# Kernel optimization log

Measured on AMD Instinct MI355X. Metric: run time of the kernel, lower is better.

## Reference

```python
import jax, jax.numpy as jnp
import numpy as np

NUM_HEADS = 16

def rotate_half(x):
    h = x.shape[-1] // 2
    return jnp.concatenate([-x[..., h:], x[..., :h]], axis=-1)

def setup_inputs() -> dict:
    key = jax.random.key(0)
    k1, k2, k3 = jax.random.split(key, 3)
    B, S, H = 2, 2048, 1024
    x = jax.random.normal(k1, (B, S, H), dtype=jnp.float32)
    W_qkv = jax.random.normal(k2, (3 * H, H), dtype=jnp.float32) * (1.0 / np.sqrt(H))
    W_proj = jax.random.normal(k3, (H, H), dtype=jnp.float32) * (1.0 / np.sqrt(H))
    return {"x": x, "W_qkv": W_qkv, "W_proj": W_proj}

def reference(x, W_qkv, W_proj):
    B, S, H = x.shape
    nH = NUM_HEADS
    hd = H // nH
    # QKV projection (bias=False): y = x @ W.T
    qkv = jnp.einsum('bsh,oh->bso', x, W_qkv)  # [B,S,3H]
    q, k, v = jnp.split(qkv, 3, axis=-1)
    def to_heads(t):
        return t.reshape(B, S, nH, hd).transpose(0, 2, 1, 3)  # [B,nH,S,hd]
    q, k, v = to_heads(q), to_heads(k), to_heads(v)
    # RoPE on first half of head_dim; freqs dim = hd//2
    half = hd // 2
    inv_freq = 1.0 / (10000.0 ** (jnp.arange(0, hd, 2, dtype=jnp.float32) / hd))  # [hd//2]
    t = jnp.arange(S, dtype=jnp.float32)
    freqs = t[:, None] * inv_freq[None, :]  # [S, hd//2]
    cos = jnp.cos(freqs)[None, None]  # [1,1,S,hd//2]
    sin = jnp.sin(freqs)[None, None]
    q_half, q_rest = q[..., :half], q[..., half:]
    k_half, k_rest = k[..., :half], k[..., half:]
    q_rot = q_half * cos + rotate_half(q_half) * sin
    k_rot = k_half * cos + rotate_half(k_half) * sin
    q = jnp.concatenate([q_rot, q_rest], axis=-1)
    k = jnp.concatenate([k_rot, k_rest], axis=-1)
    # scaled dot-product attention (no mask, dropout=0 / eval)
    scale = 1.0 / np.sqrt(hd)
    att = jnp.einsum('bhqd,bhkd->bhqk', q, k) * scale  # [B,nH,S,S]
    att = jax.nn.softmax(att, axis=-1)
    out = jnp.einsum('bhqk,bhkd->bhqd', att, v)  # [B,nH,S,hd]
    out = out.transpose(0, 2, 1, 3).reshape(B, S, H)
    return jnp.einsum('bsh,oh->bso', out, W_proj)
```

## Files before the change

### kernel.cpp

```cpp
#include <hip/hip_runtime.h>
#include <math.h>

#define SEQ  2048
#define NHD  16
#define HD   64
#define HDIM 1024

typedef short s16x8 __attribute__((ext_vector_type(8)));
typedef short s16x4 __attribute__((ext_vector_type(4)));
typedef float f32x4 __attribute__((ext_vector_type(4)));

typedef const __attribute__((address_space(1))) unsigned int* gp_t;
typedef __attribute__((address_space(3))) unsigned int* lp_t;

__device__ __forceinline__ void async16(const short* g, short* l) {
    __builtin_amdgcn_global_load_lds((gp_t)g, (lp_t)l, 16, 0, 0);
}

__device__ __forceinline__ short f2bf(float f) {
    unsigned int u = __float_as_uint(f);
    u += 0x7fff + ((u >> 16) & 1);
    return (short)(u >> 16);
}
__device__ __forceinline__ float bf2f(short s) {
    return __uint_as_float(((unsigned int)(unsigned short)s) << 16);
}
__device__ __forceinline__ unsigned pkbf(float a, float b) {
    unsigned ua = __float_as_uint(a) + 0x8000u;
    unsigned ub = __float_as_uint(b) + 0x8000u;
    return __builtin_amdgcn_perm(ua, ub, 0x03020706u);
}

#define XG4  (4096 * 1024 / 4)
#define WQG4 (3072 * 1024 / 4)
#define WPG4 (1024 * 1024 / 4)
#define NCVT ((XG4 + WQG4 + WPG4) / 256)
__global__ void cvt_rope_k(const void* __restrict__ xr, const void* __restrict__ wqr,
                           const void* __restrict__ wpr, short* __restrict__ xo,
                           short* __restrict__ wqo, short* __restrict__ wpo,
                           float2* __restrict__ tab) {
    const int tid = threadIdx.x;
    if (blockIdx.x >= NCVT) {
        int i = (blockIdx.x - NCVT) * 256 + tid;
        int s = i >> 5, d = i & 31;
        float invf = (float)pow(10000.0, -(double)d / 32.0);
        float af = (float)s * invf;
        tab[i] = make_float2((float)cos((double)af), (float)sin((double)af));
        return;
    }
    int i = blockIdx.x * 256 + tid;
    const void* in; short* out; int j;
    if (i < XG4)             { in = xr;  out = xo;  j = i; }
    else if (i < XG4 + WQG4) { in = wqr; out = wqo; j = i - XG4; }
    else                     { in = wpr; out = wpo; j = i - XG4 - WQG4; }
    const int jbase = j - tid;
    unsigned short h = ((const unsigned short*)in)[(size_t)jbase * 4 + tid];
    int e = (h >> 7) & 0xFF;
    unsigned long long b = __ballot(e >= 100 && e <= 140);
    __shared__ int tot;
    if (tid == 0) tot = 0;
    __syncthreads();
    if ((tid & 63) == 0) atomicAdd(&tot, __popcll(b));
    __syncthreads();
    if (tot > 230) {
        ((s16x4*)out)[j] = ((const s16x4*)in)[j];
    } else {
        f32x4 v = ((const f32x4*)in)[j];
        union { unsigned u[2]; s16x4 v; } r;
        r.u[0] = pkbf(v[0], v[1]);
        r.u[1] = pkbf(v[2], v[3]);
        ((s16x4*)out)[j] = r.v;
    }
}

template<int MODE>
__global__ __launch_bounds__(256, 2)
void gemm_bt(const short* __restrict__ A, const short* __restrict__ B,
             short* __restrict__ q, short* __restrict__ kbuf, short* __restrict__ vt,
             float* __restrict__ C, const float2* __restrict__ tab,
             int K, int N) {
    __shared__ __align__(16) short As[2][128 * 32];
    __shared__ __align__(16) short Bs[2][128 * 32];
    const int tid  = threadIdx.x;
    const int w    = tid >> 6, lane = tid & 63;
    const int quad = lane >> 4, l16 = lane & 15;
    const int wm = (w >> 1) * 64, wn = (w & 1) * 64;
    const int rowA0 = blockIdx.y * 128;
    const int colB0 = blockIdx.x * 128;

    auto stage = [&](int buf, int kb) {
        #pragma unroll
        for (int i = 0; i < 2; ++i) {
            int cidx = i * 256 + w * 64 + lane;
            int row = cidx >> 2, sc = cidx & 3;
            int c = sc ^ (row & 3);
            async16(&A[(long)(rowA0 + row) * K + kb + c * 8],
                    &As[buf][(i * 256 + w * 64) * 8]);
            async16(&B[(long)(colB0 + row) * K + kb + c * 8],
                    &Bs[buf][(i * 256 + w * 64) * 8]);
        }
    };

    f32x4 acc[4][4] = {};
    stage(0, 0);

    for (int kb = 0, it = 0; kb < K; kb += 32, ++it) {
        const int cur = it & 1;
        __syncthreads();
        if (kb + 32 < K) stage(cur ^ 1, kb + 32);

        s16x8 af[4], bfr[4];
        const int slot = quad ^ (l16 & 3);
        #pragma unroll
        for (int mi = 0; mi < 4; ++mi)
            af[mi] = *(const s16x8*)&As[cur][(wm + mi * 16 + l16) * 32 + slot * 8];
        #pragma unroll
        for (int ni = 0; ni < 4; ++ni)
            bfr[ni] = *(const s16x8*)&Bs[cur][(wn + ni * 16 + l16) * 32 + slot * 8];
        #pragma unroll
        for (int mi = 0; mi < 4; ++mi)
            #pragma unroll
            for (int ni = 0; ni < 4; ++ni)
                acc[mi][ni] = __builtin_amdgcn_mfma_f32_16x16x32_bf16(
                    af[mi], bfr[ni], acc[mi][ni], 0, 0, 0);
    }

    const int cb = colB0 + wn;
    if (MODE == 1) {
        #pragma unroll
        for (int mi = 0; mi < 4; ++mi) {
            #pragma unroll
            for (int r = 0; r < 4; ++r) {
                int gm = rowA0 + wm + mi * 16 + quad * 4 + r;
                float* cp = C + (long)gm * N + cb + l16;
                #pragma unroll
                for (int ni = 0; ni < 4; ++ni)
                    cp[ni * 16] = acc[mi][ni][r];
            }
        }
        return;
    }
    const int sector = cb >> 10;
    const int head   = (cb & 1023) >> 6;
    const int gmb = rowA0 + wm;
    const int b = gmb >> 11, s0 = gmb & 2047;
    __syncthreads();
    short* arena = (w < 2) ? (&As[0][0] + w * 4096) : (&Bs[0][0] + (w - 2) * 4096);
    auto aw = [&](int row, int col, short val) {
        arena[row * 64 + (((col >> 3) ^ (row & 7)) << 3) + (col & 7)] = val;
    };
    if (sector < 2) {
        const float sc = (sector == 0) ? 0.18033688f : 1.0f;
        #pragma unroll
        for (int mi = 0; mi < 4; ++mi) {
            #pragma unroll
            for (int r = 0; r < 4; ++r) {
                int lrow = mi * 16 + quad * 4 + r;
                int s = s0 + lrow;
                float v0 = acc[mi][0][r], v1 = acc[mi][1][r];
                float v2 = acc[mi][2][r], v3 = acc[mi][3][r];
                float2 cs0 = tab[s * 32 + l16];
                float2 cs1 = tab[s * 32 + 16 + l16];
                float n0 = v0 * cs0.x - v1 * cs0.y;
                float n1 = v1 * cs1.x + v0 * cs1.y;
                aw(lrow, l16,      f2bf(n0 * sc));
                aw(lrow, l16 + 16, f2bf(n1 * sc));
                aw(lrow, l16 + 32, f2bf(v2 * sc));
                aw(lrow, l16 + 48, f2bf(v3 * sc));
            }
        }
        short* dst0 = (sector == 0 ? q : kbuf)
                    + ((long)((b * NHD + head) * SEQ + s0)) * HD;
        #pragma unroll
        for (int it = 0; it < 8; ++it) {
            int row = it * 8 + (lane >> 3), cc = lane & 7;
            s16x8 vv = *(const s16x8*)&arena[row * 64 + ((cc ^ (row & 7)) << 3)];
            *(s16x8*)&dst0[row * HD + cc * 8] = vv;
        }
    } else {
        #pragma unroll
        for (int mi = 0; mi < 4; ++mi) {
            #pragma unroll
            for (int r = 0; r < 4; ++r) {
                int scol = mi * 16 + quad * 4 + r;
                aw(l16,      scol, f2bf(acc[mi][0][r]));
                aw(l16 + 16, scol, f2bf(acc[mi][1][r]));
                aw(l16 + 32, scol, f2bf(acc[mi][2][r]));
                aw(l16 + 48, scol, f2bf(acc[mi][3][r]));
            }
        }
        short* dstv = vt + ((long)((b * NHD + head) * HD)) * SEQ + s0;
        #pragma unroll
        for (int it = 0; it < 8; ++it) {
            int dd = it * 8 + (lane >> 3), so8 = lane & 7;
            s16x8 vv = *(const s16x8*)&arena[dd * 64 + ((so8 ^ (dd & 7)) << 3)];
            *(s16x8*)&dstv[(long)dd * SEQ + so8 * 8] = vv;
        }
    }
}

__global__ __launch_bounds__(256, 4)
void flash_attn(const short* __restrict__ Q, const short* __restrict__ K,
                const short* __restrict__ Vt, short* __restrict__ opart,
                float* __restrict__ lpart, int nt) {
    __shared__ __align__(16) short Ks[2][64 * 64];
    __shared__ __align__(16) short Vs[2][64 * 64];
    const int tid  = threadIdx.x;
    const int w    = tid >> 6, lane = tid & 63;
    const int quad = lane >> 4, l16 = lane & 15;
    const int bh = blockIdx.x >> 1;
    const int z  = blockIdx.x & 1;
    const int qb = blockIdx.y * 128;
    const short* Qp = Q  + (long)bh * SEQ * HD + (long)qb * HD;
    const short* Kp = K  + (long)bh * SEQ * HD;
    const short* Vp = Vt + (long)bh * HD * SEQ;
    const int kt0 = z * nt;

    auto stage = [&](int buf, int kt) {
        #pragma unroll
        for (int i = 0; i < 2; ++i) {
            int cidx = i * 256 + w * 64 + lane;
            int row = cidx >> 3, sc = cidx & 7;
            int c = sc ^ (row & 7);
            async16(&Kp[(kt * 64 + row) * HD + c * 8],
                    &Ks[buf][(i * 256 + w * 64) * 8]);
            async16(&Vp[(long)row * SEQ + kt * 64 + c * 8],
                    &Vs[buf][(i * 256 + w * 64) * 8]);
        }
    };

    s16x8 aq[2][2];
    #pragma unroll
    for (int mi = 0; mi < 2; ++mi)
        #pragma unroll
        for (int ks = 0; ks < 2; ++ks)
            aq[mi][ks] = *(const s16x8*)&Qp[(w * 32 + mi * 16 + l16) * HD
                                            + ks * 32 + quad * 8];

    s16x8 ones8;
    #pragma unroll
    for (int j = 0; j < 8; ++j) ones8[j] = (short)0x3F80;

    const f32x4 z4 = {};
    f32x4 oacc[2][4] = {};
    f32x4 lacc[2] = {};

    stage(0, kt0);
    for (int it = 0; it < nt; ++it) {
        const int cur = it & 1;
        __syncthreads();
        if (it + 1 < nt) stage(cur ^ 1, kt0 + it + 1);
        const short* kcur = Ks[cur];
        const short* vcur = Vs[cur];

        f32x4 st[2][4];
        #pragma unroll
        for (int ki = 0; ki < 4; ++ki) {
            s16x8 ak0 = *(const s16x8*)&kcur[(ki * 16 + l16) * 64 + (quad ^ (l16 & 7)) * 8];
            s16x8 ak1 = *(const s16x8*)&kcur[(ki * 16 + l16) * 64 + ((4 + quad) ^ (l16 & 7)) * 8];
            #pragma unroll
            for (int mi = 0; mi < 2; ++mi) {
                st[mi][ki] = __builtin_amdgcn_mfma_f32_16x16x32_bf16(
                    ak0, aq[mi][0], z4, 0, 0, 0);
                st[mi][ki] = __builtin_amdgcn_mfma_f32_16x16x32_bf16(
                    ak1, aq[mi][1], st[mi][ki], 0, 0, 0);
            }
        }

        s16x8 bp[2][2];
        #pragma unroll
        for (int mi = 0; mi < 2; ++mi)
            #pragma unroll
            for (int t = 0; t < 2; ++t) {
                union { unsigned u[4]; s16x8 v; } pk;
                pk.u[0] = pkbf(__builtin_amdgcn_exp2f(st[mi][2 * t][0]),
                               __builtin_amdgcn_exp2f(st[mi][2 * t][1]));
                pk.u[1] = pkbf(__builtin_amdgcn_exp2f(st[mi][2 * t][2]),
                               __builtin_amdgcn_exp2f(st[mi][2 * t][3]));
                pk.u[2] = pkbf(__builtin_amdgcn_exp2f(st[mi][2 * t + 1][0]),
                               __builtin_amdgcn_exp2f(st[mi][2 * t + 1][1]));
                pk.u[3] = pkbf(__builtin_amdgcn_exp2f(st[mi][2 * t + 1][2]),
                               __builtin_amdgcn_exp2f(st[mi][2 * t + 1][3]));
                bp[mi][t] = pk.v;
            }

        #pragma unroll
        for (int t = 0; t < 2; ++t) {
            #pragma unroll
            for (int nd = 0; nd < 4; ++nd) {
                int d = nd * 16 + l16;
                s16x4 va = *(const s16x4*)&vcur[d * 64
                             + ((4 * t + (quad >> 1)) ^ (l16 & 7)) * 8
                             + (quad & 1) * 4];
                s16x4 vb = *(const s16x4*)&vcur[d * 64
                             + ((4 * t + 2 + (quad >> 1)) ^ (l16 & 7)) * 8
                             + (quad & 1) * 4];
                s16x8 av = {va[0], va[1], va[2], va[3],
                            vb[0], vb[1], vb[2], vb[3]};
                #pragma unroll
                for (int mi = 0; mi < 2; ++mi)
                    oacc[mi][nd] = __builtin_amdgcn_mfma_f32_16x16x32_bf16(
                        av, bp[mi][t], oacc[mi][nd], 0, 0, 0);
            }
            #pragma unroll
            for (int mi = 0; mi < 2; ++mi)
                lacc[mi] = __builtin_amdgcn_mfma_f32_16x16x32_bf16(
                    ones8, bp[mi][t], lacc[mi], 0, 0, 0);
        }
    }

    #pragma unroll
    for (int mi = 0; mi < 2; ++mi) {
        int srow = qb + w * 32 + mi * 16 + l16;
        long prow = (long)(z * 2 * NHD + bh) * SEQ + srow;
        if (quad == 0) lpart[prow] = lacc[mi][0];
        short* op = opart + prow * 64 + quad * 4;
        #pragma unroll
        for (int nd = 0; nd < 4; ++nd) {
            union { unsigned u[2]; s16x4 v; } pk;
            pk.u[0] = pkbf(oacc[mi][nd][0], oacc[mi][nd][1]);
            pk.u[1] = pkbf(oacc[mi][nd][2], oacc[mi][nd][3]);
            *(s16x4*)&op[nd * 16] = pk.v;
        }
    }
}

__global__ __launch_bounds__(256)
void merge_k(const short* __restrict__ opart, const float* __restrict__ lpart,
             short* __restrict__ att) {
    int idx = blockIdx.x * 256 + threadIdx.x;
    int t16 = idx & 15, rowg = idx >> 4;
    int bh = rowg >> 11, srow = rowg & 2047;
    float inv = 1.0f / (lpart[rowg] + lpart[65536 + rowg]);
    s16x4 o1 = *(const s16x4*)&opart[(long)rowg * 64 + t16 * 4];
    s16x4 o2 = *(const s16x4*)&opart[(long)(65536 + rowg) * 64 + t16 * 4];
    int b = bh >> 4, h = bh & 15;
    short* dst = att + ((long)(b * SEQ + srow)) * HDIM + h * HD + t16 * 4;
    union { unsigned u[2]; s16x4 v; } r;
    r.u[0] = pkbf((bf2f(o1[0]) + bf2f(o2[0])) * inv,
                  (bf2f(o1[1]) + bf2f(o2[1])) * inv);
    r.u[1] = pkbf((bf2f(o1[2]) + bf2f(o2[2])) * inv,
                  (bf2f(o1[3]) + bf2f(o2[3])) * inv);
    *(s16x4*)dst = r.v;
}

extern "C" void kernel_launch(void* const* d_in, const int* in_sizes, int n_in,
                              void* d_out, int out_size, void* d_ws, size_t ws_size,
                              hipStream_t stream) {
    const void* x_raw  = d_in[0];
    const void* Wq_raw = d_in[1];
    const void* Wp_raw = d_in[2];
    for (int i = 0; i < n_in; ++i) {
        if      (in_sizes[i] == 4096 * 1024) x_raw  = d_in[i];
        else if (in_sizes[i] == 3072 * 1024) Wq_raw = d_in[i];
        else if (in_sizes[i] == 1024 * 1024) Wp_raw = d_in[i];
    }
    float* out = (float*)d_out;

    const size_t MB = 1u << 20;
    char* ws = (char*)d_ws;
    short*  q     = (short*)(ws);
    short*  k     = (short*)(ws +  8 * MB);
    short*  vt    = (short*)(ws + 16 * MB);
    short*  xbf   = (short*)(ws + 24 * MB);
    short*  att   = xbf;
    short*  wqkv  = (short*)(ws + 32 * MB);
    short*  wprj  = (short*)(ws + 38 * MB);
    float2* tab   = (float2*)(ws + 40 * MB);
    short*  opart = (short*)(ws + 41 * MB);
    float*  lprt  = (float*)(ws + 57 * MB);

    cvt_rope_k<<<dim3(NCVT + SEQ * 32 / 256), dim3(256), 0, stream>>>(
        x_raw, Wq_raw, Wp_raw, xbf, wqkv, wprj, tab);

    gemm_bt<0><<<dim3(3072 / 128, 4096 / 128), dim3(256), 0, stream>>>(
        xbf, wqkv, q, k, vt, (float*)nullptr, tab, 1024, 3072);

    flash_attn<<<dim3(2 * NHD * 2, SEQ / 128), dim3(256), 0, stream>>>(
        q, k, vt, opart, lprt, 16);

    merge_k<<<dim3(65536 * 16 / 256), dim3(256), 0, stream>>>(opart, lprt, att);

    gemm_bt<1><<<dim3(1024 / 128, 4096 / 128), dim3(256), 0, stream>>>(
        att, wprj, (short*)nullptr, (short*)nullptr, (short*)nullptr, out, tab, 1024, 1024);
}
```

Before: 191.3 us.

## Fuse split-K attention merge into output projection GEMM A-tile staging

Removes the separate merge kernel and instead combines the two flash-attention partial outputs and normalises them by their summed row sums while staging the A tiles of the output projection GEMM. This avoids one kernel launch and a full write and re-read of the merged attention tensor. The projection GEMM now uses 64-row tiles, which doubles the block count, and A staging uses synchronous global loads with arithmetic instead of async LDS loads. That can expose load latency, and the merge work is repeated once for each of the 8 column blocks.

```diff
diff --git a/kernel.cpp b/kernel.cpp
--- a/kernel.cpp
+++ b/kernel.cpp
@@ -73,12 +73,10 @@
     }
 }
 
-template<int MODE>
 __global__ __launch_bounds__(256, 2)
-void gemm_bt(const short* __restrict__ A, const short* __restrict__ B,
-             short* __restrict__ q, short* __restrict__ kbuf, short* __restrict__ vt,
-             float* __restrict__ C, const float2* __restrict__ tab,
-             int K, int N) {
+void gemm_qkv(const short* __restrict__ A, const short* __restrict__ B,
+              short* __restrict__ q, short* __restrict__ kbuf, short* __restrict__ vt,
+              const float2* __restrict__ tab, int K) {
     __shared__ __align__(16) short As[2][128 * 32];
     __shared__ __align__(16) short Bs[2][128 * 32];
     const int tid  = threadIdx.x;
@@ -126,20 +124,6 @@
     }
 
     const int cb = colB0 + wn;
-    if (MODE == 1) {
-        #pragma unroll
-        for (int mi = 0; mi < 4; ++mi) {
-            #pragma unroll
-            for (int r = 0; r < 4; ++r) {
-                int gm = rowA0 + wm + mi * 16 + quad * 4 + r;
-                float* cp = C + (long)gm * N + cb + l16;
-                #pragma unroll
-                for (int ni = 0; ni < 4; ++ni)
-                    cp[ni * 16] = acc[mi][ni][r];
-            }
-        }
-        return;
-    }
     const int sector = cb >> 10;
     const int head   = (cb & 1023) >> 6;
     const int gmb = rowA0 + wm;
@@ -325,23 +309,85 @@
     }
 }
 
-__global__ __launch_bounds__(256)
-void merge_k(const short* __restrict__ opart, const float* __restrict__ lpart,
-             short* __restrict__ att) {
-    int idx = blockIdx.x * 256 + threadIdx.x;
-    int t16 = idx & 15, rowg = idx >> 4;
-    int bh = rowg >> 11, srow = rowg & 2047;
-    float inv = 1.0f / (lpart[rowg] + lpart[65536 + rowg]);
-    s16x4 o1 = *(const s16x4*)&opart[(long)rowg * 64 + t16 * 4];
-    s16x4 o2 = *(const s16x4*)&opart[(long)(65536 + rowg) * 64 + t16 * 4];
-    int b = bh >> 4, h = bh & 15;
-    short* dst = att + ((long)(b * SEQ + srow)) * HDIM + h * HD + t16 * 4;
-    union { unsigned u[2]; s16x4 v; } r;
-    r.u[0] = pkbf((bf2f(o1[0]) + bf2f(o2[0])) * inv,
-                  (bf2f(o1[1]) + bf2f(o2[1])) * inv);
-    r.u[1] = pkbf((bf2f(o1[2]) + bf2f(o2[2])) * inv,
-                  (bf2f(o1[3]) + bf2f(o2[3])) * inv);
-    *(s16x4*)dst = r.v;
+__global__ __launch_bounds__(256, 2)
+void gemm_proj(const short* __restrict__ opart, const float* __restrict__ lpart,
+               const short* __restrict__ B, float* __restrict__ C) {
+    __shared__ __align__(16) short As[2][64 * 32];
+    __shared__ __align__(16) short Bs[2][128 * 32];
+    const int tid  = threadIdx.x;
+    const int w    = tid >> 6, lane = tid & 63;
+    const int quad = lane >> 4, l16 = lane & 15;
+    const int wm = (w >> 1) * 32, wn = (w & 1) * 64;
+    const int rowA0 = blockIdx.y * 64;
+    const int colB0 = blockIdx.x * 128;
+
+    auto stageB = [&](int buf, int kb) {
+        #pragma unroll
+        for (int i = 0; i < 2; ++i) {
+            int cidx = i * 256 + w * 64 + lane;
+            int row = cidx >> 2, sc = cidx & 3;
+            int c = sc ^ (row & 3);
+            async16(&B[(long)(colB0 + row) * HDIM + kb + c * 8],
+                    &Bs[buf][(i * 256 + w * 64) * 8]);
+        }
+    };
+    auto stageA = [&](int buf, int kb) {
+        int cidx = w * 64 + lane;
+        int row = cidx >> 2, sc = cidx & 3;
+        int c = sc ^ (row & 3);
+        int col = kb + c * 8;
+        int h = col >> 6, d = col & 63;
+        int gm = rowA0 + row;
+        int b = gm >> 11, s = gm & 2047;
+        long prow = (long)(b * NHD + h) * SEQ + s;
+        s16x8 o1 = *(const s16x8*)&opart[prow * 64 + d];
+        s16x8 o2 = *(const s16x8*)&opart[(prow + 65536) * 64 + d];
+        float inv = 1.0f / (lpart[prow] + lpart[prow + 65536]);
+        union { unsigned u[4]; s16x8 v; } pk;
+        #pragma unroll
+        for (int j = 0; j < 4; ++j)
+            pk.u[j] = pkbf((bf2f(o1[2 * j])     + bf2f(o2[2 * j]))     * inv,
+                           (bf2f(o1[2 * j + 1]) + bf2f(o2[2 * j + 1])) * inv);
+        *(s16x8*)&As[buf][(row * 4 + sc) * 8] = pk.v;
+    };
+
+    f32x4 acc[2][4] = {};
+    stageB(0, 0);
+    stageA(0, 0);
+
+    for (int kb = 0, it = 0; kb < HDIM; kb += 32, ++it) {
+        const int cur = it & 1;
+        __syncthreads();
+        if (kb + 32 < HDIM) { stageB(cur ^ 1, kb + 32); stageA(cur ^ 1, kb + 32); }
+
+        s16x8 af[2], bfr[4];
+        const int slot = quad ^ (l16 & 3);
+        #pragma unroll
+        for (int mi = 0; mi < 2; ++mi)
+            af[mi] = *(const s16x8*)&As[cur][(wm + mi * 16 + l16) * 32 + slot * 8];
+        #pragma unroll
+        for (int ni = 0; ni < 4; ++ni)
+            bfr[ni] = *(const s16x8*)&Bs[cur][(wn + ni * 16 + l16) * 32 + slot * 8];
+        #pragma unroll
+        for (int mi = 0; mi < 2; ++mi)
+            #pragma unroll
+            for (int ni = 0; ni < 4; ++ni)
+                acc[mi][ni] = __builtin_amdgcn_mfma_f32_16x16x32_bf16(
+                    af[mi], bfr[ni], acc[mi][ni], 0, 0, 0);
+    }
+
+    const int cb = colB0 + wn;
+    #pragma unroll
+    for (int mi = 0; mi < 2; ++mi) {
+        #pragma unroll
+        for (int r = 0; r < 4; ++r) {
+            int gm = rowA0 + wm + mi * 16 + quad * 4 + r;
+            float* cp = C + (long)gm * HDIM + cb + l16;
+            #pragma unroll
+            for (int ni = 0; ni < 4; ++ni)
+                cp[ni * 16] = acc[mi][ni][r];
+        }
+    }
 }
 
 extern "C" void kernel_launch(void* const* d_in, const int* in_sizes, int n_in,
@@ -363,7 +409,6 @@
     short*  k     = (short*)(ws +  8 * MB);
     short*  vt    = (short*)(ws + 16 * MB);
     short*  xbf   = (short*)(ws + 24 * MB);
-    short*  att   = xbf;
     short*  wqkv  = (short*)(ws + 32 * MB);
     short*  wprj  = (short*)(ws + 38 * MB);
     float2* tab   = (float2*)(ws + 40 * MB);
@@ -373,14 +418,12 @@
     cvt_rope_k<<<dim3(NCVT + SEQ * 32 / 256), dim3(256), 0, stream>>>(
         x_raw, Wq_raw, Wp_raw, xbf, wqkv, wprj, tab);
 
-    gemm_bt<0><<<dim3(3072 / 128, 4096 / 128), dim3(256), 0, stream>>>(
-        xbf, wqkv, q, k, vt, (float*)nullptr, tab, 1024, 3072);
+    gemm_qkv<<<dim3(3072 / 128, 4096 / 128), dim3(256), 0, stream>>>(
+        xbf, wqkv, q, k, vt, tab, 1024);
 
     flash_attn<<<dim3(2 * NHD * 2, SEQ / 128), dim3(256), 0, stream>>>(
         q, k, vt, opart, lprt, 16);
 
-    merge_k<<<dim3(65536 * 16 / 256), dim3(256), 0, stream>>>(opart, lprt, att);
-
-    gemm_bt<1><<<dim3(1024 / 128, 4096 / 128), dim3(256), 0, stream>>>(
-        att, wprj, (short*)nullptr, (short*)nullptr, (short*)nullptr, out, tab, 1024, 1024);
-}
+    gemm_proj<<<dim3(1024 / 128, 4096 / 64), dim3(256), 0, stream>>>(
+        opart, lprt, wprj, out);
+}
```

Result: no change. 192.2 us (+0.5%).
